# Kernel optimization log

Hardware: AMD Instinct MI355X
Metric: run time of the kernel (lower is better)

Reference implementation:

```python
import jax, jax.numpy as jnp
import numpy as np

DIM = 256
HEADS = 8
DIM_HEAD = 64
HIDDEN = HEADS * DIM_HEAD
B, H, W = 8, 64, 64


def setup_inputs() -> dict:
    key = jax.random.key(0)
    ks = jax.random.split(key, 7)
    x = jax.random.normal(ks[0], (B, DIM, H, W), dtype=jnp.float32)
    norm_w = jnp.ones((DIM,), jnp.float32)
    w_qkv = jax.random.normal(ks[1], (3 * HIDDEN, DIM), jnp.float32) * (1.0 / np.sqrt(DIM))
    mem_kv = jax.random.normal(ks[2], (2, HEADS, DIM_HEAD, HEADS), jnp.float32)
    w_out = jax.random.normal(ks[3], (DIM, HIDDEN), jnp.float32) * (1.0 / np.sqrt(HIDDEN))
    b_out = jnp.zeros((DIM,), jnp.float32)
    out_norm_w = jnp.ones((DIM,), jnp.float32)
    return {"x": x, "norm_w": norm_w, "w_qkv": w_qkv, "mem_kv": mem_kv,
            "w_out": w_out, "b_out": b_out, "out_norm_w": out_norm_w}


def _rms2d(t, w, dim):
    # F.normalize(t, dim=1) * weight * sqrt(dim)
    n = jnp.sqrt(jnp.sum(t * t, axis=1, keepdims=True))
    return t / jnp.maximum(n, 1e-12) * w[None, :, None, None] * (dim ** 0.5)


def reference(x, norm_w, w_qkv, mem_kv, w_out, b_out, out_norm_w):
    b, c, hh, ww = x.shape
    heads = mem_kv.shape[1]
    dh = mem_kv.shape[2]
    n = hh * ww
    xn = _rms2d(x, norm_w, c)
    # 1x1 conv, no bias: [b, 3*hidden, h, w]
    qkv = jnp.einsum('bchw,oc->bohw', xn, w_qkv)
    q, k, v = jnp.split(qkv, 3, axis=1)
    q = q.reshape(b, heads, dh, n)
    k = k.reshape(b, heads, dh, n)
    v = v.reshape(b, heads, dh, n)
    mk = jnp.broadcast_to(mem_kv[0][None], (b, heads, dh, mem_kv.shape[3]))
    mv = jnp.broadcast_to(mem_kv[1][None], (b, heads, dh, mem_kv.shape[3]))
    k = jnp.concatenate([mk, k], axis=-1)
    v = jnp.concatenate([mv, v], axis=-1)
    q = jax.nn.softmax(q, axis=-2) * (dh ** -0.5)
    k = jax.nn.softmax(k, axis=-1)
    context = jnp.einsum('bhdn,bhen->bhde', k, v)
    out = jnp.einsum('bhde,bhdn->bhen', context, q)
    out = out.reshape(b, heads * dh, hh, ww)
    out = jnp.einsum('bchw,oc->bohw', out, w_out) + b_out[None, :, None, None]
    return _rms2d(out, out_norm_w, c)
```

## Files before the change

kernel.cpp:

```cpp
#include <hip/hip_runtime.h>
#include <math.h>

#define NB 8
#define NC 256
#define NPIX 4096
#define NO3 1536
#define NHID 512
#define NHEADS 8
#define NDH 64

typedef unsigned short u16;
typedef __attribute__((ext_vector_type(8))) short short8;
typedef __attribute__((ext_vector_type(4))) float f32x4;

#define WS_KMAX  0
#define WS_KSUM  4096
#define WS_CTXP  8192
#define WS_WQBF  1056768
#define WS_WOBF  1253376
#define WS_QKV   1318912

__device__ __forceinline__ u16 f2bf(float f) {
    unsigned u = __builtin_bit_cast(unsigned, f);
    unsigned r = (u + 0x7FFFu + ((u >> 16) & 1u)) >> 16;
    return (u16)r;
}

typedef const __attribute__((address_space(1))) unsigned int guint;
typedef __attribute__((address_space(3))) unsigned int luint;

__global__ __launch_bounds__(256) void k_scale_convert(const float* __restrict__ x,
                                                        const float* __restrict__ norm_w,
                                                        u16* __restrict__ xbfT) {
    __shared__ float xs[64][257];
    __shared__ float red[4][64];
    __shared__ float ssh[64];
    int blk = blockIdx.x;
    int b = blk >> 6;
    int n0 = (blk & 63) * 64;
    const float* xb = x + (size_t)b * NC * NPIX;
    int t = threadIdx.x;
    int p = t & 63, q = t >> 6;
    float accv = 0.f;
    #pragma unroll 8
    for (int c = q * 64; c < q * 64 + 64; ++c) {
        float v = xb[(size_t)c * NPIX + n0 + p];
        xs[p][c] = v;
        accv = fmaf(v, v, accv);
    }
    red[q][p] = accv;
    __syncthreads();
    if (t < 64) {
        float sum = red[0][t] + red[1][t] + red[2][t] + red[3][t];
        ssh[t] = 16.0f / fmaxf(sqrtf(sum), 1e-12f);
    }
    __syncthreads();
    int p2 = t >> 2, cbase = (t & 3) * 64;
    float sc = ssh[p2];
    u16* orow = xbfT + (size_t)(b * NPIX + n0 + p2) * NC + cbase;
    #pragma unroll
    for (int j = 0; j < 64; j += 8) {
        union { u16 us[8]; uint4 v; } pk;
        #pragma unroll
        for (int u = 0; u < 8; ++u)
            pk.us[u] = f2bf(xs[p2][cbase + j + u] * norm_w[cbase + j + u] * sc);
        *(uint4*)(orow + j) = pk.v;
    }
}

__global__ __launch_bounds__(256) void k_wconv(const float* __restrict__ wq, const float* __restrict__ wo,
                                                u16* __restrict__ wqbf, u16* __restrict__ wobf) {
    int idx = blockIdx.x * 256 + threadIdx.x;
    int e = idx * 4;
    if (e < 393216) {
        float4 v = *(const float4*)(wq + e);
        union { u16 us[4]; uint2 v2; } pk;
        pk.us[0] = f2bf(v.x); pk.us[1] = f2bf(v.y); pk.us[2] = f2bf(v.z); pk.us[3] = f2bf(v.w);
        *(uint2*)(wqbf + e) = pk.v2;
    } else {
        int e2 = e - 393216;
        float4 v = *(const float4*)(wo + e2);
        union { u16 us[4]; uint2 v2; } pk;
        pk.us[0] = f2bf(v.x); pk.us[1] = f2bf(v.y); pk.us[2] = f2bf(v.z); pk.us[3] = f2bf(v.w);
        *(uint2*)(wobf + e2) = pk.v2;
    }
}

template<int KD, bool BIAS>
__global__ __launch_bounds__(256) void k_mfma_nt(const u16* __restrict__ A, const u16* __restrict__ B,
                                                  const float* __restrict__ bias, float* __restrict__ C,
                                                  size_t bStride, size_t cStride) {
    __shared__ u16 lA[128 * 64];
    __shared__ u16 lB[128 * 64];
    const int b = blockIdx.z;
    const int m0 = blockIdx.y * 128;
    const int n0 = blockIdx.x * 128;
    const u16* Bb = B + (size_t)b * bStride;
    float* Cb = C + (size_t)b * cStride;
    const int t = threadIdx.x;
    const int lane = t & 63;
    const int wid = t >> 6;
    const int wr = (wid >> 1) * 64;
    const int wc = (wid & 1) * 64;
    const int fr = lane & 15;
    const int fq = lane >> 4;

    f32x4 acc[4][4];
    #pragma unroll
    for (int i = 0; i < 4; ++i)
        #pragma unroll
        for (int j = 0; j < 4; ++j) acc[i][j] = (f32x4){0.f, 0.f, 0.f, 0.f};

    for (int k0 = 0; k0 < KD; k0 += 64) {
        #pragma unroll
        for (int i = 0; i < 4; ++i) {
            int idx = i * 256 + t;
            int row = idx >> 3;
            int col = (idx & 7) * 8;
            __builtin_amdgcn_global_load_lds((guint*)(A + (size_t)(m0 + row) * KD + k0 + col),
                                             (luint*)(&lA[idx * 8]), 16, 0, 0);
            __builtin_amdgcn_global_load_lds((guint*)(Bb + (size_t)(n0 + row) * KD + k0 + col),
                                             (luint*)(&lB[idx * 8]), 16, 0, 0);
        }
        __syncthreads();
        #pragma unroll
        for (int kk = 0; kk < 2; ++kk) {
            short8 af[4], bfv[4];
            #pragma unroll
            for (int i = 0; i < 4; ++i)
                af[i] = *(const short8*)&lA[(wr + i * 16 + fr) * 64 + kk * 32 + fq * 8];
            #pragma unroll
            for (int j = 0; j < 4; ++j)
                bfv[j] = *(const short8*)&lB[(wc + j * 16 + fr) * 64 + kk * 32 + fq * 8];
            #pragma unroll
            for (int i = 0; i < 4; ++i)
                #pragma unroll
                for (int j = 0; j < 4; ++j)
                    acc[i][j] = __builtin_amdgcn_mfma_f32_16x16x32_bf16(af[i], bfv[j], acc[i][j], 0, 0, 0);
        }
        __syncthreads();
    }
    #pragma unroll
    for (int i = 0; i < 4; ++i) {
        int rbase = m0 + wr + i * 16 + fq * 4;
        #pragma unroll
        for (int j = 0; j < 4; ++j) {
            int c = n0 + wc + j * 16 + fr;
            #pragma unroll
            for (int r = 0; r < 4; ++r) {
                float v = acc[i][j][r];
                if (BIAS) v += bias[rbase + r];
                Cb[(size_t)(rbase + r) * NPIX + c] = v;
            }
        }
    }
}

__global__ __launch_bounds__(256) void k_q_softmax(float* __restrict__ qkv) {
    int idx = blockIdx.x * 256 + threadIdx.x;
    int n = idx & 4095;
    int bh = idx >> 12;
    int b = bh >> 3, h = bh & 7;
    float* qp = qkv + ((size_t)b * NO3 + h * NDH) * NPIX + n;
    float v[64];
    float mx = -1e30f;
    #pragma unroll
    for (int d = 0; d < 64; ++d) { v[d] = qp[(size_t)d * NPIX]; mx = fmaxf(mx, v[d]); }
    float sum = 0.f;
    #pragma unroll
    for (int d = 0; d < 64; ++d) { v[d] = __expf(v[d] - mx); sum += v[d]; }
    float inv = 0.125f / sum;
    #pragma unroll
    for (int d = 0; d < 64; ++d) qp[(size_t)d * NPIX] = v[d] * inv;
}

__global__ __launch_bounds__(256) void k_k_stats(const float* __restrict__ qkv, const float* __restrict__ mem_kv,
                                                 float* __restrict__ kmax, float* __restrict__ ksum) {
    int row = blockIdx.x;
    int b = row >> 9, hd = row & 511;
    int h = hd >> 6, d = hd & 63;
    const float* kp = qkv + ((size_t)b * NO3 + NHID + hd) * NPIX;
    int t = threadIdx.x;
    float m = -1e30f, sum = 0.f;
    for (int n = t; n < NPIX; n += 256) {
        float v = kp[n];
        if (v > m) { sum *= __expf(m - v); m = v; }
        sum += __expf(v - m);
    }
    if (t < 8) {
        float v = mem_kv[((size_t)h * 64 + d) * 8 + t];
        if (v > m) { sum *= __expf(m - v); m = v; }
        sum += __expf(v - m);
    }
    __shared__ float sm[256], ss[256];
    sm[t] = m; ss[t] = sum;
    __syncthreads();
    for (int st = 128; st > 0; st >>= 1) {
        if (t < st) {
            float m1 = sm[t], m2 = sm[t + st];
            float s1 = ss[t], s2 = ss[t + st];
            float mm = fmaxf(m1, m2);
            sm[t] = mm;
            ss[t] = s1 * __expf(m1 - mm) + s2 * __expf(m2 - mm);
        }
        __syncthreads();
    }
    if (t == 0) { kmax[row] = sm[0]; ksum[row] = ss[0]; }
}

__global__ __launch_bounds__(256) void k_context(const float* __restrict__ qkv, const float* __restrict__ mem_kv,
                                                 const float* __restrict__ kmax, const float* __restrict__ ksum,
                                                 float* __restrict__ ctxp) {
    int bh = blockIdx.x;
    int p = blockIdx.y;
    int b = bh >> 3, h = bh & 7;
    const float* kp = qkv + ((size_t)b * NO3 + NHID + h * NDH) * NPIX;
    const float* vp = qkv + ((size_t)b * NO3 + 2 * NHID + h * NDH) * NPIX;
    __shared__ float KsT[64][68];
    __shared__ float VsT[64][68];
    __shared__ float smx[64], sinv[64];
    int t = threadIdx.x;
    if (t < 64) { smx[t] = kmax[bh * 64 + t]; sinv[t] = 1.0f / ksum[bh * 64 + t]; }
    __syncthreads();
    int tx = t & 15, ty = t >> 4;
    int d0 = ty * 4, e0 = tx * 4;
    float acc[4][4] = {{0.f}};
    if (p == 0) {
        const float* mkp = mem_kv + (size_t)h * 64 * 8;
        const float* mvp = mem_kv + (size_t)NHEADS * 64 * 8 + (size_t)h * 64 * 8;
        #pragma unroll
        for (int j = 0; j < 8; ++j) {
            float vv[4];
            #pragma unroll
            for (int q = 0; q < 4; ++q) vv[q] = mvp[(e0 + q) * 8 + j];
            #pragma unroll
            for (int i = 0; i < 4; ++i) {
                float kk = __expf(mkp[(d0 + i) * 8 + j] - smx[d0 + i]) * sinv[d0 + i];
                #pragma unroll
                for (int q = 0; q < 4; ++q) acc[i][q] = fmaf(kk, vv[q], acc[i][q]);
            }
        }
    }
    int rr = t >> 6, cc = t & 63;
    for (int n0 = p * 1024; n0 < p * 1024 + 1024; n0 += 64) {
        #pragma unroll
        for (int i = 0; i < 16; ++i) {
            int row = rr + i * 4;
            float kv = kp[(size_t)row * NPIX + n0 + cc];
            KsT[cc][row] = __expf(kv - smx[row]) * sinv[row];
            VsT[cc][row] = vp[(size_t)row * NPIX + n0 + cc];
        }
        __syncthreads();
        #pragma unroll 4
        for (int n = 0; n < 64; ++n) {
            float4 a = *(const float4*)&KsT[n][d0];
            float4 vv = *(const float4*)&VsT[n][e0];
            float av[4] = {a.x, a.y, a.z, a.w};
            float vvv[4] = {vv.x, vv.y, vv.z, vv.w};
            #pragma unroll
            for (int i = 0; i < 4; ++i)
                #pragma unroll
                for (int q = 0; q < 4; ++q) acc[i][q] = fmaf(av[i], vvv[q], acc[i][q]);
        }
        __syncthreads();
    }
    #pragma unroll
    for (int i = 0; i < 4; ++i)
        #pragma unroll
        for (int q = 0; q < 4; ++q)
            ctxp[(((size_t)p * 64 + bh) * 64 + d0 + i) * 64 + e0 + q] = acc[i][q];
}

__global__ __launch_bounds__(256) void k_pv(float* __restrict__ qkv, const float* __restrict__ ctxp) {
    int nb = blockIdx.x;
    int bh = blockIdx.y;
    int b = bh >> 3, h = bh & 7;
    __shared__ float Cs[64][64];
    int t = threadIdx.x;
    for (int i = t; i < 4096; i += 256) {
        float v = 0.f;
        #pragma unroll
        for (int p = 0; p < 4; ++p) v += ctxp[((size_t)p * 64 + bh) * 4096 + i];
        Cs[i >> 6][i & 63] = v;
    }
    __syncthreads();
    int n = nb * 256 + t;
    const float* qp = qkv + ((size_t)b * NO3 + h * NDH) * NPIX + n;
    float acc[64];
    #pragma unroll
    for (int e = 0; e < 64; ++e) acc[e] = 0.f;
    #pragma unroll 2
    for (int d = 0; d < 64; ++d) {
        float qv = qp[(size_t)d * NPIX];
        const float4* crow = (const float4*)&Cs[d][0];
        #pragma unroll
        for (int e4 = 0; e4 < 16; ++e4) {
            float4 cv = crow[e4];
            acc[e4 * 4 + 0] = fmaf(cv.x, qv, acc[e4 * 4 + 0]);
            acc[e4 * 4 + 1] = fmaf(cv.y, qv, acc[e4 * 4 + 1]);
            acc[e4 * 4 + 2] = fmaf(cv.z, qv, acc[e4 * 4 + 2]);
            acc[e4 * 4 + 3] = fmaf(cv.w, qv, acc[e4 * 4 + 3]);
        }
    }
    u16* outT = (u16*)(qkv + ((size_t)b * NO3 + NHID) * NPIX);
    u16* op = outT + (size_t)n * NHID + h * NDH;
    #pragma unroll
    for (int e8 = 0; e8 < 8; ++e8) {
        union { u16 us[8]; uint4 v; } pk;
        #pragma unroll
        for (int u = 0; u < 8; ++u) pk.us[u] = f2bf(acc[e8 * 8 + u]);
        *(uint4*)(op + e8 * 8) = pk.v;
    }
}

__global__ __launch_bounds__(256) void k_out_norm(float* __restrict__ out, const float* __restrict__ onw) {
    int idx = blockIdx.x * 256 + threadIdx.x;
    int b = idx >> 12, n = idx & 4095;
    float* op = out + (size_t)b * NC * NPIX + n;
    float acc = 0.f;
    #pragma unroll 8
    for (int c = 0; c < NC; ++c) { float v = op[(size_t)c * NPIX]; acc = fmaf(v, v, acc); }
    float sc = 16.0f / fmaxf(sqrtf(acc), 1e-12f);
    #pragma unroll 8
    for (int c = 0; c < NC; ++c) op[(size_t)c * NPIX] = op[(size_t)c * NPIX] * (sc * onw[c]);
}

extern "C" void kernel_launch(void* const* d_in, const int* in_sizes, int n_in,
                              void* d_out, int out_size, void* d_ws, size_t ws_size,
                              hipStream_t stream) {
    const float* x      = (const float*)d_in[0];
    const float* norm_w = (const float*)d_in[1];
    const float* w_qkv  = (const float*)d_in[2];
    const float* mem_kv = (const float*)d_in[3];
    const float* w_out  = (const float*)d_in[4];
    const float* b_out  = (const float*)d_in[5];
    const float* onw    = (const float*)d_in[6];
    float* out = (float*)d_out;
    float* ws  = (float*)d_ws;

    float* kmax = ws + WS_KMAX;
    float* ksum = ws + WS_KSUM;
    float* ctxp = ws + WS_CTXP;
    u16*   wqbf = (u16*)(ws + WS_WQBF);
    u16*   wobf = (u16*)(ws + WS_WOBF);
    float* qkv  = ws + WS_QKV;
    u16*   xbfT = (u16*)d_out;
    const u16* outT = (const u16*)(qkv + (size_t)NHID * NPIX);

    k_wconv        <<<dim3(512),          dim3(256), 0, stream>>>(w_qkv, w_out, wqbf, wobf);
    k_scale_convert<<<dim3(NB * 64),      dim3(256), 0, stream>>>(x, norm_w, xbfT);
    k_mfma_nt<256, false><<<dim3(32, 12, NB), dim3(256), 0, stream>>>(
        wqbf, xbfT, nullptr, qkv, (size_t)NPIX * NC, (size_t)NO3 * NPIX);
    k_q_softmax    <<<dim3(NB * NHEADS * NPIX / 256), dim3(256), 0, stream>>>(qkv);
    k_k_stats      <<<dim3(NB * NHID),    dim3(256), 0, stream>>>(qkv, mem_kv, kmax, ksum);
    k_context      <<<dim3(NB * NHEADS, 4), dim3(256), 0, stream>>>(qkv, mem_kv, kmax, ksum, ctxp);
    k_pv           <<<dim3(16, NB * NHEADS), dim3(256), 0, stream>>>(qkv, ctxp);
    k_mfma_nt<512, true><<<dim3(32, 2, NB), dim3(256), 0, stream>>>(
        wobf, outT, b_out, out, (size_t)NO3 * NPIX * 2, (size_t)NC * NPIX);
    k_out_norm     <<<dim3(NB * NPIX / 256), dim3(256), 0, stream>>>(out, onw);
}
```

Baseline: 341.2 us.

## Fuse q softmax into pv and split context over 16 partitions

Removes the standalone q-softmax kernel and computes the softmax over d inside k_pv on values already loaded into registers. This avoids one full read-modify-write pass over q in global memory. The context kernel now splits the sequence into 16 partitions instead of 4, giving 1024 blocks rather than 256 for more parallelism. The partial sums are stored in spare output memory and combined by a new reduce kernel, at the cost of one extra launch and more partial-sum traffic.

```diff
diff --git a/kernel.cpp b/kernel.cpp
--- a/kernel.cpp
+++ b/kernel.cpp
@@ -8,6 +8,7 @@
 #define NHID 512
 #define NHEADS 8
 #define NDH 64
+#define NPART 16
 
 typedef unsigned short u16;
 typedef __attribute__((ext_vector_type(8))) short short8;
@@ -15,7 +16,7 @@
 
 #define WS_KMAX  0
 #define WS_KSUM  4096
-#define WS_CTXP  8192
+#define WS_CTX   8192
 #define WS_WQBF  1056768
 #define WS_WOBF  1253376
 #define WS_QKV   1318912
@@ -156,24 +157,6 @@
     }
 }
 
-__global__ __launch_bounds__(256) void k_q_softmax(float* __restrict__ qkv) {
-    int idx = blockIdx.x * 256 + threadIdx.x;
-    int n = idx & 4095;
-    int bh = idx >> 12;
-    int b = bh >> 3, h = bh & 7;
-    float* qp = qkv + ((size_t)b * NO3 + h * NDH) * NPIX + n;
-    float v[64];
-    float mx = -1e30f;
-    #pragma unroll
-    for (int d = 0; d < 64; ++d) { v[d] = qp[(size_t)d * NPIX]; mx = fmaxf(mx, v[d]); }
-    float sum = 0.f;
-    #pragma unroll
-    for (int d = 0; d < 64; ++d) { v[d] = __expf(v[d] - mx); sum += v[d]; }
-    float inv = 0.125f / sum;
-    #pragma unroll
-    for (int d = 0; d < 64; ++d) qp[(size_t)d * NPIX] = v[d] * inv;
-}
-
 __global__ __launch_bounds__(256) void k_k_stats(const float* __restrict__ qkv, const float* __restrict__ mem_kv,
                                                  float* __restrict__ kmax, float* __restrict__ ksum) {
     int row = blockIdx.x;
@@ -242,7 +225,7 @@
         }
     }
     int rr = t >> 6, cc = t & 63;
-    for (int n0 = p * 1024; n0 < p * 1024 + 1024; n0 += 64) {
+    for (int n0 = p * 256; n0 < p * 256 + 256; n0 += 64) {
         #pragma unroll
         for (int i = 0; i < 16; ++i) {
             int row = rr + i * 4;
@@ -271,35 +254,47 @@
             ctxp[(((size_t)p * 64 + bh) * 64 + d0 + i) * 64 + e0 + q] = acc[i][q];
 }
 
-__global__ __launch_bounds__(256) void k_pv(float* __restrict__ qkv, const float* __restrict__ ctxp) {
+__global__ __launch_bounds__(256) void k_ctx_reduce(const float* __restrict__ ctxp, float* __restrict__ ctx) {
+    int idx = blockIdx.x * 256 + threadIdx.x;
+    float s = 0.f;
+    #pragma unroll
+    for (int p = 0; p < NPART; ++p) s += ctxp[(size_t)p * 262144 + idx];
+    ctx[idx] = s;
+}
+
+__global__ __launch_bounds__(256) void k_pv(float* __restrict__ qkv, const float* __restrict__ ctx) {
     int nb = blockIdx.x;
     int bh = blockIdx.y;
     int b = bh >> 3, h = bh & 7;
     __shared__ float Cs[64][64];
     int t = threadIdx.x;
-    for (int i = t; i < 4096; i += 256) {
-        float v = 0.f;
-        #pragma unroll
-        for (int p = 0; p < 4; ++p) v += ctxp[((size_t)p * 64 + bh) * 4096 + i];
-        Cs[i >> 6][i & 63] = v;
-    }
+    for (int i = t; i < 4096; i += 256)
+        Cs[i >> 6][i & 63] = ctx[(size_t)bh * 4096 + i];
     __syncthreads();
     int n = nb * 256 + t;
     const float* qp = qkv + ((size_t)b * NO3 + h * NDH) * NPIX + n;
+    float qv[64];
+    float mx = -1e30f;
+    #pragma unroll
+    for (int d = 0; d < 64; ++d) { qv[d] = qp[(size_t)d * NPIX]; mx = fmaxf(mx, qv[d]); }
+    float sum = 0.f;
+    #pragma unroll
+    for (int d = 0; d < 64; ++d) { qv[d] = __expf(qv[d] - mx); sum += qv[d]; }
+    float inv = 0.125f / sum;
     float acc[64];
     #pragma unroll
     for (int e = 0; e < 64; ++e) acc[e] = 0.f;
     #pragma unroll 2
     for (int d = 0; d < 64; ++d) {
-        float qv = qp[(size_t)d * NPIX];
+        float w = qv[d] * inv;
         const float4* crow = (const float4*)&Cs[d][0];
         #pragma unroll
         for (int e4 = 0; e4 < 16; ++e4) {
             float4 cv = crow[e4];
-            acc[e4 * 4 + 0] = fmaf(cv.x, qv, acc[e4 * 4 + 0]);
-            acc[e4 * 4 + 1] = fmaf(cv.y, qv, acc[e4 * 4 + 1]);
-            acc[e4 * 4 + 2] = fmaf(cv.z, qv, acc[e4 * 4 + 2]);
-            acc[e4 * 4 + 3] = fmaf(cv.w, qv, acc[e4 * 4 + 3]);
+            acc[e4 * 4 + 0] = fmaf(cv.x, w, acc[e4 * 4 + 0]);
+            acc[e4 * 4 + 1] = fmaf(cv.y, w, acc[e4 * 4 + 1]);
+            acc[e4 * 4 + 2] = fmaf(cv.z, w, acc[e4 * 4 + 2]);
+            acc[e4 * 4 + 3] = fmaf(cv.w, w, acc[e4 * 4 + 3]);
         }
     }
     u16* outT = (u16*)(qkv + ((size_t)b * NO3 + NHID) * NPIX);
@@ -340,21 +335,22 @@
 
     float* kmax = ws + WS_KMAX;
     float* ksum = ws + WS_KSUM;
-    float* ctxp = ws + WS_CTXP;
+    float* ctx  = ws + WS_CTX;
     u16*   wqbf = (u16*)(ws + WS_WQBF);
     u16*   wobf = (u16*)(ws + WS_WOBF);
     float* qkv  = ws + WS_QKV;
-    u16*   xbfT = (u16*)d_out;
+    u16*   xbfT  = (u16*)d_out;
+    float* ctxp  = (float*)d_out + 4194304;
     const u16* outT = (const u16*)(qkv + (size_t)NHID * NPIX);
 
-    k_wconv        <<<dim3(512),          dim3(256), 0, stream>>>(w_qkv, w_out, wqbf, wobf);
-    k_scale_convert<<<dim3(NB * 64),      dim3(256), 0, stream>>>(x, norm_w, xbfT);
+    k_wconv        <<<dim3(512),            dim3(256), 0, stream>>>(w_qkv, w_out, wqbf, wobf);
+    k_scale_convert<<<dim3(NB * 64),        dim3(256), 0, stream>>>(x, norm_w, xbfT);
     k_mfma_nt<256, false><<<dim3(32, 12, NB), dim3(256), 0, stream>>>(
         wqbf, xbfT, nullptr, qkv, (size_t)NPIX * NC, (size_t)NO3 * NPIX);
-    k_q_softmax    <<<dim3(NB * NHEADS * NPIX / 256), dim3(256), 0, stream>>>(qkv);
-    k_k_stats      <<<dim3(NB * NHID),    dim3(256), 0, stream>>>(qkv, mem_kv, kmax, ksum);
-    k_context      <<<dim3(NB * NHEADS, 4), dim3(256), 0, stream>>>(qkv, mem_kv, kmax, ksum, ctxp);
-    k_pv           <<<dim3(16, NB * NHEADS), dim3(256), 0, stream>>>(qkv, ctxp);
+    k_k_stats      <<<dim3(NB * NHID),      dim3(256), 0, stream>>>(qkv, mem_kv, kmax, ksum);
+    k_context      <<<dim3(NB * NHEADS, NPART), dim3(256), 0, stream>>>(qkv, mem_kv, kmax, ksum, ctxp);
+    k_ctx_reduce   <<<dim3(1024),           dim3(256), 0, stream>>>(ctxp, ctx);
+    k_pv           <<<dim3(16, NB * NHEADS), dim3(256), 0, stream>>>(qkv, ctx);
     k_mfma_nt<512, true><<<dim3(32, 2, NB), dim3(256), 0, stream>>>(
         wobf, outT, b_out, out, (size_t)NO3 * NPIX * 2, (size_t)NC * NPIX);
     k_out_norm     <<<dim3(NB * NPIX / 256), dim3(256), 0, stream>>>(out, onw);
```

Result: faster. 333.6 us (-2.2%).
